# Kernel tuning notes

Measured on AMD Instinct MI355X. Metric: run time of the kernel, lower is better.

Reference implementation:

```python
import jax, jax.numpy as jnp
import numpy as np

B, T, I, H, K, C, TH, CLS = 128, 512, 300, 150, 6, 300, 20, 5

def setup_inputs() -> dict:
    key = jax.random.key(0)
    ks = jax.random.split(key, 16)
    s = lambda *sh: 1.0 / np.sqrt(sh[-1])
    inp = {
        "x": jax.random.normal(ks[0], (B, T, I), jnp.float32),
        # GRU params (PyTorch layout: [3H, in]) for fwd/bwd directions
        "Wih_f": jax.random.normal(ks[1], (3 * H, I), jnp.float32) * s(3 * H, I),
        "Whh_f": jax.random.normal(ks[2], (3 * H, H), jnp.float32) * s(3 * H, H),
        "bih_f": jax.random.normal(ks[3], (3 * H,), jnp.float32) * 0.01,
        "bhh_f": jax.random.normal(ks[4], (3 * H,), jnp.float32) * 0.01,
        "Wih_b": jax.random.normal(ks[5], (3 * H, I), jnp.float32) * s(3 * H, I),
        "Whh_b": jax.random.normal(ks[6], (3 * H, H), jnp.float32) * s(3 * H, H),
        "bih_b": jax.random.normal(ks[7], (3 * H,), jnp.float32) * 0.01,
        "bhh_b": jax.random.normal(ks[8], (3 * H,), jnp.float32) * 0.01,
        # topic attention params (stacked over K topics)
        "attn_context": jax.random.normal(ks[9], (K, C), jnp.float32),
        "Wattn": jax.random.normal(ks[10], (K, C + 2 * H, 2 * H), jnp.float32) * s(1, C + 2 * H),
        "battn": jax.random.normal(ks[11], (K, 2 * H), jnp.float32) * 0.01,
        "Wtop": jax.random.normal(ks[12], (K, 2 * H, TH), jnp.float32) * s(1, 2 * H),
        "btop": jax.random.normal(ks[13], (K, TH), jnp.float32) * 0.01,
        "Wout": jax.random.normal(ks[14], (K * TH, CLS), jnp.float32) * s(1, K * TH),
        "bout": jax.random.normal(ks[15], (CLS,), jnp.float32) * 0.01,
    }
    return inp

def _gru_dir(x, Wih, Whh, bih, bhh, reverse):
    # x: [B,T,I] -> outputs [B,T,H], final hidden [B,H]
    xT = jnp.swapaxes(x, 0, 1)                    # [T,B,I]
    if reverse:
        xT = xT[::-1]
    gi = xT @ Wih.T + bih                         # [T,B,3H] input projections (one big GEMM)
    h0 = jnp.zeros((x.shape[0], Whh.shape[1]), x.dtype)
    def step(h, g):
        gh = h @ Whh.T + bhh
        i_r, i_z, i_n = jnp.split(g, 3, axis=-1)
        h_r, h_z, h_n = jnp.split(gh, 3, axis=-1)
        r = jax.nn.sigmoid(i_r + h_r)
        z = jax.nn.sigmoid(i_z + h_z)
        n = jnp.tanh(i_n + r * h_n)
        h_new = (1.0 - z) * n + z * h
        return h_new, h_new
    hT, ys = jax.lax.scan(step, h0, gi)
    if reverse:
        ys = ys[::-1]
    return jnp.swapaxes(ys, 0, 1), hT

def reference(x, Wih_f, Whh_f, bih_f, bhh_f, Wih_b, Whh_b, bih_b, bhh_b,
              attn_context, Wattn, battn, Wtop, btop, Wout, bout):
    # eval mode: dropout is identity
    out_f, h_f = _gru_dir(x, Wih_f, Whh_f, bih_f, bhh_f, False)
    out_b, h_b = _gru_dir(x, Wih_b, Whh_b, bih_b, bhh_b, True)
    seq = jnp.concatenate([out_f, out_b], axis=-1)       # [B,T,2H]
    hidden = jnp.concatenate([h_f, h_b], axis=-1)        # [B,2H]
    Bsz = x.shape[0]
    Kt = attn_context.shape[0]
    # per-topic context: cat(context_k, hidden) -> linear -> tanh, batched over topics
    ctx_in = jnp.concatenate([
        jnp.broadcast_to(attn_context[None, :, :], (Bsz, Kt, attn_context.shape[1])),
        jnp.broadcast_to(hidden[:, None, :], (Bsz, Kt, hidden.shape[1])),
    ], axis=-1)                                          # [B,K,C+2H]
    context = jnp.tanh(jnp.einsum('bkc,kcd->bkd', ctx_in, Wattn) + battn)  # [B,K,2H]
    # attention pooling over time, all topics at once
    energy = jnp.einsum('btd,bkd->btk', seq, context)    # [B,T,K]
    probs = jax.nn.softmax(energy, axis=1)
    pooled = jnp.einsum('btd,btk->bkd', seq, probs)      # [B,K,2H]
    topic = jax.nn.relu(jnp.einsum('bkd,kdh->bkh', pooled, Wtop) + btop)   # [B,K,TH]
    feats = topic.reshape(Bsz, -1)                       # [B,K*TH]
    logits = feats @ Wout + bout
    out = jax.nn.softmax(logits, axis=1)                 # eval + validate=False path
    # regularization loss on normalized contexts
    nc = context / jnp.linalg.norm(context, axis=2, keepdims=True).clip(1e-12)
    G = jnp.einsum('bkd,bjd->bkj', nc, nc)               # [B,K,K]
    diff = G - jnp.eye(Kt, dtype=G.dtype)[None]
    reg = jnp.mean(jnp.sqrt(jnp.sum(diff * diff, axis=(1, 2))))
    return out, reg
```

## Files before the change

### kernel.cpp

```cpp
#include <hip/hip_runtime.h>
#include <hip/hip_bf16.h>
#include <math.h>

#define Bq   128
#define Tq   512
#define Iq   300
#define Hq   150
#define G3   450
#define Kq   6
#define Cq   300
#define D2   300
#define THq  20
#define CLSq 5

typedef __attribute__((ext_vector_type(8))) short short8;
typedef __attribute__((ext_vector_type(4))) float floatx4;

__global__ __launch_bounds__(256) void cast_bf16_kernel(
    const float* __restrict__ in, __hip_bfloat16* __restrict__ out, int n4)
{
    const int i = blockIdx.x * 256 + threadIdx.x;
    if (i < n4) {
        float4 v = *(const float4*)(in + 4 * (size_t)i);
        out[4 * (size_t)i + 0] = __float2bfloat16(v.x);
        out[4 * (size_t)i + 1] = __float2bfloat16(v.y);
        out[4 * (size_t)i + 2] = __float2bfloat16(v.z);
        out[4 * (size_t)i + 3] = __float2bfloat16(v.w);
    }
}

#define LB 40

__global__ __launch_bounds__(256) void gi_gemm_mfma(
    const __hip_bfloat16* __restrict__ xb,
    const __hip_bfloat16* __restrict__ Wbf,
    const float* __restrict__ bf_, const float* __restrict__ bb_,
    float* __restrict__ gic, int t0f, int t0b, int tcShift)
{
    const int dir = blockIdx.z;
    const unsigned short* W = (const unsigned short*)(Wbf + (size_t)dir * G3 * Iq);
    const unsigned short* X = (const unsigned short*)xb;
    const float* bias = dir ? bb_ : bf_;
    const int t0 = dir ? t0b : t0f;
    const int TCr = 1 << tcShift;
    float* outb = gic + (size_t)dir * Bq * TCr * G3;

    const int m0 = blockIdx.y * 128;
    const int n0 = blockIdx.x * 128;
    const int tid  = threadIdx.x;
    const int wv   = tid >> 6, lane = tid & 63;
    const int wm   = wv & 1,  wn   = wv >> 1;
    const int quad = lane >> 4, mr = lane & 15;

    __shared__ __align__(16) unsigned short Ab[128 * LB];
    __shared__ __align__(16) unsigned short Bb[128 * LB];

    floatx4 acc[4][4];
    #pragma unroll
    for (int i = 0; i < 4; ++i)
        #pragma unroll
        for (int j = 0; j < 4; ++j)
            acc[i][j] = (floatx4){0.f, 0.f, 0.f, 0.f};

    for (int k0 = 0; k0 < 320; k0 += 32) {
        __syncthreads();
        #pragma unroll
        for (int i = 0; i < 4; ++i) {
            const int g = tid + 256 * i;
            const int row = g >> 3, kq = g & 7;
            const int k = k0 + kq * 4;
            const int r = m0 + row;
            const int bb2 = r >> tcShift, lt = r & (TCr - 1);
            ushort4 av = make_ushort4(0, 0, 0, 0);
            if (k < Iq)
                av = *(const ushort4*)(X + ((size_t)bb2 * Tq + t0 + lt) * Iq + k);
            *(ushort4*)&Ab[row * LB + kq * 4] = av;
            const int n = n0 + row;
            ushort4 bv = make_ushort4(0, 0, 0, 0);
            if (n < G3 && k < Iq)
                bv = *(const ushort4*)(W + (size_t)n * Iq + k);
            *(ushort4*)&Bb[row * LB + kq * 4] = bv;
        }
        __syncthreads();

        short8 af[4], bfr[4];
        #pragma unroll
        for (int i = 0; i < 4; ++i)
            af[i] = *(const short8*)&Ab[(wm * 64 + i * 16 + mr) * LB + quad * 8];
        #pragma unroll
        for (int j = 0; j < 4; ++j)
            bfr[j] = *(const short8*)&Bb[(wn * 64 + j * 16 + mr) * LB + quad * 8];
        #pragma unroll
        for (int i = 0; i < 4; ++i)
            #pragma unroll
            for (int j = 0; j < 4; ++j)
                acc[i][j] = __builtin_amdgcn_mfma_f32_16x16x32_bf16(
                    af[i], bfr[j], acc[i][j], 0, 0, 0);
    }

    #pragma unroll
    for (int j = 0; j < 4; ++j) {
        const int gn = n0 + wn * 64 + j * 16 + mr;
        if (gn >= G3) continue;
        const float bv = bias[gn];
        #pragma unroll
        for (int i = 0; i < 4; ++i) {
            const int mbase = m0 + wm * 64 + i * 16 + quad * 4;
            #pragma unroll
            for (int rg = 0; rg < 4; ++rg)
                outb[(size_t)(mbase + rg) * G3 + gn] = acc[i][j][rg] + bv;
        }
    }
}

__global__ __launch_bounds__(512, 2) void gru_rec(
    const float* __restrict__ gic,
    const float* __restrict__ Whh_f, const float* __restrict__ bhh_f,
    const float* __restrict__ Whh_b, const float* __restrict__ bhh_b,
    float* __restrict__ hstate,
    float* __restrict__ seq,
    int chunk, int tcShift)
{
    const int TCr = 1 << tcShift;
    const int bid = blockIdx.x;
    const int dir = bid & 1;
    const int b   = bid >> 1;
    const float* Whh = dir ? Whh_b : Whh_f;
    const float* bhh = dir ? bhh_b : bhh_f;
    const int tid = threadIdx.x;
    const int j2  = tid >> 1;
    const int p   = tid & 1;
    const bool gact = (tid < 450);

    __shared__ __align__(16) float stage[64 * 150];
    __shared__ __align__(16) float4 hbuf4[38];
    __shared__ float gh_s[456];
    __shared__ float gi_s[456];
    float* hbuf = (float*)hbuf4;

    float w0[76], w1[76];

    for (int c = 0; c < 8; ++c) {
        const int r0 = c * 64;
        const int nrows = (r0 + 64 <= G3) ? 64 : (G3 - r0);
        const int nel = nrows * 150;
        __syncthreads();
        for (int idx = tid * 4; idx < nel; idx += 512 * 4)
            *(float4*)&stage[idx] = *(const float4*)(Whh + (size_t)r0 * 150 + idx);
        __syncthreads();
        if (gact && (j2 >> 5) == c) {
            const int rl = 2 * j2 - r0;
            #pragma unroll
            for (int m = 0; m < 75; ++m) {
                w0[m] = stage[rl * 150 + p * 75 + m];
                w1[m] = stage[(rl + 1) * 150 + p * 75 + m];
            }
        }
    }
    w0[75] = 0.f; w1[75] = 0.f;
    const float bh0 = (gact && p == 0) ? bhh[2 * j2]     : 0.f;
    const float bh1 = (gact && p == 0) ? bhh[2 * j2 + 1] : 0.f;

    float* hs = hstate + (size_t)(dir * Bq + b) * Hq;
    if (tid < 152) {
        const int pp = tid / 76, mm = tid % 76;
        hbuf[tid] = (mm < 75 && chunk > 0) ? hs[pp * 75 + mm] : 0.f;
    }
    __syncthreads();

    const float* gib = gic + (size_t)(dir * Bq + b) * TCr * G3;
    const int t0 = dir ? (Tq - TCr * (chunk + 1)) : (chunk * TCr);
    float* seqb = seq + (size_t)b * Tq * D2 + dir * Hq;

    int lt = dir ? (TCr - 1) : 0;
    float gval = gact ? gib[(size_t)lt * G3 + tid] : 0.f;

    for (int s = 0; s < TCr; ++s) {
        const int ltn = dir ? (TCr - 2 - s) : (s + 1);
        float gnext = 0.f;
        if (s + 1 < TCr && gact)
            gnext = gib[(size_t)ltn * G3 + tid];

        if (gact) {
            float a0a = 0.f, a0b = 0.f, a1a = 0.f, a1b = 0.f;
            const float4* hh = hbuf4 + p * 19;
            #pragma unroll
            for (int q = 0; q < 19; q += 2) {
                float4 hv = hh[q];
                a0a += hv.x * w0[q*4+0] + hv.y * w0[q*4+1]
                     + hv.z * w0[q*4+2] + hv.w * w0[q*4+3];
                a1a += hv.x * w1[q*4+0] + hv.y * w1[q*4+1]
                     + hv.z * w1[q*4+2] + hv.w * w1[q*4+3];
            }
            #pragma unroll
            for (int q = 1; q < 19; q += 2) {
                float4 hv = hh[q];
                a0b += hv.x * w0[q*4+0] + hv.y * w0[q*4+1]
                     + hv.z * w0[q*4+2] + hv.w * w0[q*4+3];
                a1b += hv.x * w1[q*4+0] + hv.y * w1[q*4+1]
                     + hv.z * w1[q*4+2] + hv.w * w1[q*4+3];
            }
            float acc0 = a0a + a0b, acc1 = a1a + a1b;
            const float o0 = __shfl_xor(acc0, 1);
            const float o1 = __shfl_xor(acc1, 1);
            if (p == 0)
                *(float2*)&gh_s[2 * j2] = make_float2(acc0 + o0 + bh0,
                                                      acc1 + o1 + bh1);
            gi_s[tid] = gval;
        }
        __syncthreads();

        if (tid < Hq) {
            const float r = 1.f / (1.f + __expf(-(gi_s[tid]       + gh_s[tid])));
            const float z = 1.f / (1.f + __expf(-(gi_s[150 + tid] + gh_s[150 + tid])));
            const float nv = tanhf(gi_s[300 + tid] + r * gh_s[300 + tid]);
            const int slot = (tid / 75) * 76 + (tid % 75);
            const float hn = (1.f - z) * nv + z * hbuf[slot];
            hbuf[slot] = hn;
            stage[(s & 63) * 150 + tid] = hn;
        }
        __syncthreads();

        if ((s & 63) == 63 || s == TCr - 1) {
            const int sf0 = s & ~63;
            const int nf2 = (s - sf0 + 1) * 75;
            for (int idx = tid; idx < nf2; idx += 512) {
                const int rrow = idx / 75, cc = idx % 75;
                const int ss = sf0 + rrow;
                const int ltw = dir ? (TCr - 1 - ss) : ss;
                *(float2*)(seqb + (size_t)(t0 + ltw) * D2 + 2 * cc) =
                    *(const float2*)&stage[rrow * 150 + 2 * cc];
            }
        }

        gval = gnext;
        lt = ltn;
    }

    if (tid < Hq) hs[tid] = hbuf[(tid / 75) * 76 + (tid % 75)];
}

__global__ void ctxw_kernel(
    const float* __restrict__ attn_context,
    const float* __restrict__ Wattn,
    const float* __restrict__ battn,
    float* __restrict__ ctxW)
{
    const int o = blockIdx.x * 256 + threadIdx.x;
    if (o >= Kq * D2) return;
    const int k = o / D2, d = o % D2;
    float acc = battn[o];
    const float* Wp = Wattn + ((size_t)k * (Cq + D2)) * D2 + d;
    for (int c = 0; c < Cq; ++c)
        acc += attn_context[k * Cq + c] * Wp[(size_t)c * D2];
    ctxW[o] = acc;
}

__global__ __launch_bounds__(256) void ctx_compute(
    const float* __restrict__ seq,
    const float* __restrict__ Wattn,
    const float* __restrict__ ctxW,
    float* __restrict__ context,
    float* __restrict__ normsq)
{
    const int b = blockIdx.x;
    const int k = blockIdx.y;
    const int tid = threadIdx.x;
    const int lane = tid & 63, wv = tid >> 6;

    __shared__ float hb[304];
    __shared__ float red[4];

    for (int i = tid; i < D2; i += 256)
        hb[i] = (i < Hq) ? seq[((size_t)b * Tq + (Tq - 1)) * D2 + i]
                         : seq[(size_t)b * Tq * D2 + i];
    __syncthreads();

    float ssq = 0.f;
    for (int d = tid; d < D2; d += 256) {
        float acc = ctxW[k * D2 + d];
        const float* Wp = Wattn + ((size_t)k * (Cq + D2) + Cq) * D2 + d;
        for (int jj = 0; jj < D2; ++jj)
            acc += hb[jj] * Wp[(size_t)jj * D2];
        const float c = tanhf(acc);
        context[((size_t)b * Kq + k) * D2 + d] = c;
        ssq += c * c;
    }
    for (int off = 32; off > 0; off >>= 1) ssq += __shfl_xor(ssq, off, 64);
    if (lane == 0) red[wv] = ssq;
    __syncthreads();
    if (tid == 0) normsq[b * Kq + k] = red[0] + red[1] + red[2] + red[3];
}

__global__ __launch_bounds__(256) void gram_kernel(
    const float* __restrict__ context,
    const float* __restrict__ normsq,
    float* __restrict__ regbuf)
{
    const int b = blockIdx.x;
    const int tid = threadIdx.x;
    __shared__ float ctx[Kq * D2];
    __shared__ float Gm[36];

    for (int o = tid; o < Kq * D2; o += 256)
        ctx[o] = context[(size_t)b * Kq * D2 + o];
    __syncthreads();

    if (tid < 36) {
        const int k = tid / 6, jj = tid % 6;
        float g = 0.f;
        for (int d = 0; d < D2; ++d)
            g += ctx[k * D2 + d] * ctx[jj * D2 + d];
        const float nk = fmaxf(sqrtf(normsq[b * Kq + k]), 1e-12f);
        const float nj = fmaxf(sqrtf(normsq[b * Kq + jj]), 1e-12f);
        g /= (nk * nj);
        const float diff = g - ((k == jj) ? 1.f : 0.f);
        Gm[tid] = diff * diff;
    }
    __syncthreads();
    if (tid == 0) {
        float s = 0.f;
        for (int i = 0; i < 36; ++i) s += Gm[i];
        regbuf[b] = sqrtf(s);
    }
}

__global__ __launch_bounds__(256) void energy_kernel(
    const float* __restrict__ seq,
    const float* __restrict__ context,
    float* __restrict__ en)
{
    const int tc = blockIdx.x;
    const int b  = blockIdx.y;
    const int tid = threadIdx.x;
    const int lane = tid & 63, wv = tid >> 6;

    __shared__ float ctx[Kq * D2];
    for (int o = tid; o < Kq * D2; o += 256)
        ctx[o] = context[(size_t)b * Kq * D2 + o];
    __syncthreads();

    const float* seqb = seq + (size_t)b * Tq * D2;
    for (int s = 0; s < 16; ++s) {
        const int tt = tc * 64 + s * 4 + wv;
        float acc[Kq] = {0.f,0.f,0.f,0.f,0.f,0.f};
        for (int d = lane; d < D2; d += 64) {
            const float sv = seqb[(size_t)tt * D2 + d];
            #pragma unroll
            for (int k = 0; k < Kq; ++k) acc[k] += sv * ctx[k * D2 + d];
        }
        #pragma unroll
        for (int k = 0; k < Kq; ++k) {
            float v = acc[k];
            for (int off = 32; off > 0; off >>= 1) v += __shfl_xor(v, off, 64);
            if (lane == 0) en[((size_t)b * Tq + tt) * Kq + k] = v;
        }
    }
}

__global__ __launch_bounds__(256) void softmax_kernel(float* __restrict__ en)
{
    const int b = blockIdx.x;
    const int tid = threadIdx.x;
    const int lane = tid & 63, wv = tid >> 6;
    __shared__ float es[Tq * Kq];
    __shared__ float red[8];

    for (int o = tid; o < Tq * Kq; o += 256)
        es[o] = en[(size_t)b * Tq * Kq + o];
    __syncthreads();

    for (int k = 0; k < Kq; ++k) {
        float m = -1e30f;
        for (int tt = tid; tt < Tq; tt += 256) m = fmaxf(m, es[tt * Kq + k]);
        for (int off = 32; off > 0; off >>= 1) m = fmaxf(m, __shfl_xor(m, off, 64));
        if (lane == 0) red[wv] = m;
        __syncthreads();
        m = fmaxf(fmaxf(red[0], red[1]), fmaxf(red[2], red[3]));
        float ssum = 0.f;
        for (int tt = tid; tt < Tq; tt += 256) {
            const float e = __expf(es[tt * Kq + k] - m);
            es[tt * Kq + k] = e;
            ssum += e;
        }
        for (int off = 32; off > 0; off >>= 1) ssum += __shfl_xor(ssum, off, 64);
        if (lane == 0) red[4 + wv] = ssum;
        __syncthreads();
        const float inv = 1.f / (red[4] + red[5] + red[6] + red[7]);
        for (int tt = tid; tt < Tq; tt += 256) es[tt * Kq + k] *= inv;
        __syncthreads();
    }

    for (int o = tid; o < Tq * Kq; o += 256)
        en[(size_t)b * Tq * Kq + o] = es[o];
}

__global__ __launch_bounds__(256) void pooledp_kernel(
    const float* __restrict__ seq,
    const float* __restrict__ en,
    float* __restrict__ partial)
{
    const int tc = blockIdx.x;
    const int b  = blockIdx.y;
    const int tid = threadIdx.x;
    const int lane = tid & 63, wv = tid >> 6;

    __shared__ float pr[64 * Kq];
    __shared__ float part[4][Kq * D2];

    if (tid < 64 * Kq / 2) {
        pr[tid]       = en[((size_t)b * Tq + tc * 64) * Kq + tid];
        pr[tid + 192] = en[((size_t)b * Tq + tc * 64) * Kq + tid + 192];
    }
    __syncthreads();

    const float* seqb = seq + (size_t)b * Tq * D2;

    float pp[Kq][5];
    #pragma unroll
    for (int k = 0; k < Kq; ++k)
        #pragma unroll
        for (int q = 0; q < 5; ++q) pp[k][q] = 0.f;

    for (int s = 0; s < 16; ++s) {
        const int tl = s * 4 + wv;
        const int tt = tc * 64 + tl;
        float prr[Kq];
        #pragma unroll
        for (int k = 0; k < Kq; ++k) prr[k] = pr[tl * Kq + k];
        #pragma unroll
        for (int q = 0; q < 5; ++q) {
            const int d = lane + q * 64;
            const float sv = (d < D2) ? seqb[(size_t)tt * D2 + d] : 0.f;
            #pragma unroll
            for (int k = 0; k < Kq; ++k) pp[k][q] += prr[k] * sv;
        }
    }
    #pragma unroll
    for (int k = 0; k < Kq; ++k)
        #pragma unroll
        for (int q = 0; q < 5; ++q) {
            const int d = lane + q * 64;
            if (d < D2) part[wv][k * D2 + d] = pp[k][q];
        }
    __syncthreads();
    float* op = partial + ((size_t)b * 8 + tc) * (Kq * D2);
    for (int o = tid; o < Kq * D2; o += 256)
        op[o] = part[0][o] + part[1][o] + part[2][o] + part[3][o];
}

__global__ __launch_bounds__(256) void final_kernel(
    const float* __restrict__ partial,
    const float* __restrict__ Wtop,
    const float* __restrict__ btop,
    const float* __restrict__ Wout,
    const float* __restrict__ bout,
    float* __restrict__ outp)
{
    const int b = blockIdx.x;
    const int tid = threadIdx.x;
    __shared__ float pooled[Kq * D2];
    __shared__ float feats[Kq * THq];
    __shared__ float lsm[8];

    for (int o = tid; o < Kq * D2; o += 256) {
        float s = 0.f;
        #pragma unroll
        for (int c = 0; c < 8; ++c)
            s += partial[((size_t)b * 8 + c) * (Kq * D2) + o];
        pooled[o] = s;
    }
    __syncthreads();

    if (tid < Kq * THq) {
        const int k = tid / THq, hh = tid % THq;
        float acc = btop[tid];
        const float* wp = Wtop + (size_t)k * D2 * THq + hh;
        for (int d = 0; d < D2; ++d)
            acc += pooled[k * D2 + d] * wp[(size_t)d * THq];
        feats[tid] = fmaxf(acc, 0.f);
    }
    __syncthreads();

    if (tid < CLSq) {
        float acc = bout[tid];
        for (int f = 0; f < Kq * THq; ++f)
            acc += feats[f] * Wout[f * CLSq + tid];
        lsm[tid] = acc;
    }
    __syncthreads();
    if (tid < CLSq) {
        float m = lsm[0];
        for (int c = 1; c < CLSq; ++c) m = fmaxf(m, lsm[c]);
        float s = 0.f;
        for (int c = 0; c < CLSq; ++c) s += __expf(lsm[c] - m);
        outp[(size_t)b * CLSq + tid] = __expf(lsm[tid] - m) / s;
    }
}

__global__ void reg_final(const float* __restrict__ regbuf, float* __restrict__ outp)
{
    const int tid = threadIdx.x;
    float v = regbuf[tid];
    for (int off = 32; off > 0; off >>= 1) v += __shfl_xor(v, off, 64);
    __shared__ float r2[2];
    if ((tid & 63) == 0) r2[tid >> 6] = v;
    __syncthreads();
    if (tid == 0) outp[Bq * CLSq] = (r2[0] + r2[1]) * (1.f / (float)Bq);
}

extern "C" void kernel_launch(void* const* d_in, const int* in_sizes, int n_in,
                              void* d_out, int out_size, void* d_ws, size_t ws_size,
                              hipStream_t stream)
{
    const float* x     = (const float*)d_in[0];
    const float* Wih_f = (const float*)d_in[1];
    const float* Whh_f = (const float*)d_in[2];
    const float* bih_f = (const float*)d_in[3];
    const float* bhh_f = (const float*)d_in[4];
    const float* Wih_b = (const float*)d_in[5];
    const float* Whh_b = (const float*)d_in[6];
    const float* bih_b = (const float*)d_in[7];
    const float* bhh_b = (const float*)d_in[8];
    const float* attn_context = (const float*)d_in[9];
    const float* Wattn = (const float*)d_in[10];
    const float* battn = (const float*)d_in[11];
    const float* Wtop  = (const float*)d_in[12];
    const float* btop  = (const float*)d_in[13];
    const float* Wout  = (const float*)d_in[14];
    const float* bout  = (const float*)d_in[15];
    float* outp = (float*)d_out;

    float* ws       = (float*)d_ws;
    float* seqv     = ws;
    float* hstate   = seqv + (size_t)Bq * Tq * D2;
    float* ctxW     = hstate + (size_t)2 * Bq * Hq;
    float* context  = ctxW + Kq * D2;
    float* regbuf   = context + (size_t)Bq * Kq * D2;
    float* normsq   = regbuf + Bq;
    float* en       = normsq + Bq * Kq;
    float* partial  = en + (size_t)Bq * Tq * Kq;
    __hip_bfloat16* xb16 = (__hip_bfloat16*)(partial + (size_t)Bq * 8 * Kq * D2);
    __hip_bfloat16* Wb16 = xb16 + (size_t)Bq * Tq * Iq;
    float* gi_chunk = (float*)(Wb16 + (size_t)2 * G3 * Iq);
    const size_t fixed_floats = (size_t)(gi_chunk - ws);

    int tcShift = 5;
    for (int sh = 8; sh >= 5; --sh) {
        size_t need = (fixed_floats + (size_t)115200 * (1 << sh)) * 4;
        if (need <= ws_size) { tcShift = sh; break; }
    }
    const int TCr = 1 << tcShift;
    const int NL = Tq / TCr;

    cast_bf16_kernel<<<dim3((Bq * Tq * Iq / 4 + 255) / 256), 256, 0, stream>>>(
        x, xb16, Bq * Tq * Iq / 4);
    cast_bf16_kernel<<<dim3((G3 * Iq / 4 + 255) / 256), 256, 0, stream>>>(
        Wih_f, Wb16, G3 * Iq / 4);
    cast_bf16_kernel<<<dim3((G3 * Iq / 4 + 255) / 256), 256, 0, stream>>>(
        Wih_b, Wb16 + (size_t)G3 * Iq, G3 * Iq / 4);

    for (int c = 0; c < NL; ++c) {
        const int t0f = c * TCr;
        const int t0b = Tq - TCr * (c + 1);
        gi_gemm_mfma<<<dim3(4, Bq * TCr / 128, 2), 256, 0, stream>>>(
            xb16, Wb16, bih_f, bih_b, gi_chunk, t0f, t0b, tcShift);
        gru_rec<<<dim3(2 * Bq), 512, 0, stream>>>(
            gi_chunk, Whh_f, bhh_f, Whh_b, bhh_b, hstate, seqv, c, tcShift);
    }

    ctxw_kernel<<<dim3((Kq * D2 + 255) / 256), 256, 0, stream>>>(
        attn_context, Wattn, battn, ctxW);
    ctx_compute<<<dim3(Bq, Kq), 256, 0, stream>>>(seqv, Wattn, ctxW, context, normsq);
    gram_kernel<<<dim3(Bq), 256, 0, stream>>>(context, normsq, regbuf);
    energy_kernel<<<dim3(8, Bq), 256, 0, stream>>>(seqv, context, en);
    softmax_kernel<<<dim3(Bq), 256, 0, stream>>>(en);
    pooledp_kernel<<<dim3(8, Bq), 256, 0, stream>>>(seqv, en, partial);
    final_kernel<<<dim3(Bq), 256, 0, stream>>>(partial, Wtop, btop, Wout, bout, outp);
    reg_final<<<dim3(1), 128, 0, stream>>>(regbuf, outp);
}
```

Before: 1.065 ms.

## Repartition GRU recurrent matvec to 8 rows x 8 column slices per thread

The recurrent h·Whh^T matvec is redistributed so each thread owns 8 gate rows over a 19-element column slice, in place of 2 rows over 75 columns. Each thread now reads 5 float4s of h from shared memory per step instead of 19, cutting LDS traffic. The cost is a 3-stage xor-shuffle reduction across 8 lanes for 8 accumulators. The hidden-state buffer layout is padded to 8 slices of 20 to match.

```diff
diff --git a/kernel.cpp b/kernel.cpp
--- a/kernel.cpp
+++ b/kernel.cpp
@@ -128,17 +128,18 @@
     const float* Whh = dir ? Whh_b : Whh_f;
     const float* bhh = dir ? bhh_b : bhh_f;
     const int tid = threadIdx.x;
-    const int j2  = tid >> 1;
-    const int p   = tid & 1;
-    const bool gact = (tid < 450);
+    const int ro  = tid >> 3;
+    const int p   = tid & 7;
+    const bool gact = (tid < 456);
+    const bool iact = (tid < 450);
 
     __shared__ __align__(16) float stage[64 * 150];
-    __shared__ __align__(16) float4 hbuf4[38];
-    __shared__ float gh_s[456];
+    __shared__ __align__(16) float4 hbuf4[40];
+    __shared__ __align__(16) float gh_s[456];
     __shared__ float gi_s[456];
     float* hbuf = (float*)hbuf4;
 
-    float w0[76], w1[76];
+    float w[8][19];
 
     for (int c = 0; c < 8; ++c) {
         const int r0 = c * 64;
@@ -148,23 +149,29 @@
         for (int idx = tid * 4; idx < nel; idx += 512 * 4)
             *(float4*)&stage[idx] = *(const float4*)(Whh + (size_t)r0 * 150 + idx);
         __syncthreads();
-        if (gact && (j2 >> 5) == c) {
-            const int rl = 2 * j2 - r0;
-            #pragma unroll
-            for (int m = 0; m < 75; ++m) {
-                w0[m] = stage[rl * 150 + p * 75 + m];
-                w1[m] = stage[(rl + 1) * 150 + p * 75 + m];
+        if (gact && (ro >> 3) == c) {
+            const int rl = 8 * ro - r0;
+            const int cmax = (p == 7) ? 17 : 19;
+            #pragma unroll
+            for (int r = 0; r < 8; ++r) {
+                const bool rv = (8 * ro + r < G3) && (rl + r < nrows);
+                #pragma unroll
+                for (int cc = 0; cc < 19; ++cc)
+                    w[r][cc] = (rv && cc < cmax)
+                             ? stage[(rl + r) * 150 + p * 19 + cc] : 0.f;
             }
         }
     }
-    w0[75] = 0.f; w1[75] = 0.f;
-    const float bh0 = (gact && p == 0) ? bhh[2 * j2]     : 0.f;
-    const float bh1 = (gact && p == 0) ? bhh[2 * j2 + 1] : 0.f;
+    float bh[8];
+    #pragma unroll
+    for (int r = 0; r < 8; ++r)
+        bh[r] = (gact && p == 0 && 8 * ro + r < G3) ? bhh[8 * ro + r] : 0.f;
 
     float* hs = hstate + (size_t)(dir * Bq + b) * Hq;
-    if (tid < 152) {
-        const int pp = tid / 76, mm = tid % 76;
-        hbuf[tid] = (mm < 75 && chunk > 0) ? hs[pp * 75 + mm] : 0.f;
+    if (tid < 160) {
+        const int pp = tid / 20, off = tid % 20;
+        const int j = pp * 19 + off;
+        hbuf[tid] = (off < 19 && j < Hq && chunk > 0) ? hs[j] : 0.f;
     }
     __syncthreads();
 
@@ -173,40 +180,49 @@
     float* seqb = seq + (size_t)b * Tq * D2 + dir * Hq;
 
     int lt = dir ? (TCr - 1) : 0;
-    float gval = gact ? gib[(size_t)lt * G3 + tid] : 0.f;
+    float gval = iact ? gib[(size_t)lt * G3 + tid] : 0.f;
 
     for (int s = 0; s < TCr; ++s) {
         const int ltn = dir ? (TCr - 2 - s) : (s + 1);
         float gnext = 0.f;
-        if (s + 1 < TCr && gact)
+        if (s + 1 < TCr && iact)
             gnext = gib[(size_t)ltn * G3 + tid];
 
+        if (iact) gi_s[tid] = gval;
+
         if (gact) {
-            float a0a = 0.f, a0b = 0.f, a1a = 0.f, a1b = 0.f;
-            const float4* hh = hbuf4 + p * 19;
-            #pragma unroll
-            for (int q = 0; q < 19; q += 2) {
-                float4 hv = hh[q];
-                a0a += hv.x * w0[q*4+0] + hv.y * w0[q*4+1]
-                     + hv.z * w0[q*4+2] + hv.w * w0[q*4+3];
-                a1a += hv.x * w1[q*4+0] + hv.y * w1[q*4+1]
-                     + hv.z * w1[q*4+2] + hv.w * w1[q*4+3];
+            const float4 hv0 = hbuf4[p * 5 + 0];
+            const float4 hv1 = hbuf4[p * 5 + 1];
+            const float4 hv2 = hbuf4[p * 5 + 2];
+            const float4 hv3 = hbuf4[p * 5 + 3];
+            const float4 hv4 = hbuf4[p * 5 + 4];
+            float acc[8];
+            #pragma unroll
+            for (int r = 0; r < 8; ++r) {
+                acc[r] = hv0.x * w[r][0]  + hv0.y * w[r][1]
+                       + hv0.z * w[r][2]  + hv0.w * w[r][3]
+                       + hv1.x * w[r][4]  + hv1.y * w[r][5]
+                       + hv1.z * w[r][6]  + hv1.w * w[r][7]
+                       + hv2.x * w[r][8]  + hv2.y * w[r][9]
+                       + hv2.z * w[r][10] + hv2.w * w[r][11]
+                       + hv3.x * w[r][12] + hv3.y * w[r][13]
+                       + hv3.z * w[r][14] + hv3.w * w[r][15]
+                       + hv4.x * w[r][16] + hv4.y * w[r][17]
+                       + hv4.z * w[r][18];
             }
             #pragma unroll
-            for (int q = 1; q < 19; q += 2) {
-                float4 hv = hh[q];
-                a0b += hv.x * w0[q*4+0] + hv.y * w0[q*4+1]
-                     + hv.z * w0[q*4+2] + hv.w * w0[q*4+3];
-                a1b += hv.x * w1[q*4+0] + hv.y * w1[q*4+1]
-                     + hv.z * w1[q*4+2] + hv.w * w1[q*4+3];
+            for (int m = 1; m < 8; m <<= 1)
+                #pragma unroll
+                for (int r = 0; r < 8; ++r)
+                    acc[r] += __shfl_xor(acc[r], m);
+            if (p == 0) {
+                float4 lo = make_float4(acc[0] + bh[0], acc[1] + bh[1],
+                                        acc[2] + bh[2], acc[3] + bh[3]);
+                float4 hi = make_float4(acc[4] + bh[4], acc[5] + bh[5],
+                                        acc[6] + bh[6], acc[7] + bh[7]);
+                *(float4*)&gh_s[8 * ro]     = lo;
+                *(float4*)&gh_s[8 * ro + 4] = hi;
             }
-            float acc0 = a0a + a0b, acc1 = a1a + a1b;
-            const float o0 = __shfl_xor(acc0, 1);
-            const float o1 = __shfl_xor(acc1, 1);
-            if (p == 0)
-                *(float2*)&gh_s[2 * j2] = make_float2(acc0 + o0 + bh0,
-                                                      acc1 + o1 + bh1);
-            gi_s[tid] = gval;
         }
         __syncthreads();
 
@@ -214,7 +230,7 @@
             const float r = 1.f / (1.f + __expf(-(gi_s[tid]       + gh_s[tid])));
             const float z = 1.f / (1.f + __expf(-(gi_s[150 + tid] + gh_s[150 + tid])));
             const float nv = tanhf(gi_s[300 + tid] + r * gh_s[300 + tid]);
-            const int slot = (tid / 75) * 76 + (tid % 75);
+            const int slot = (tid / 19) * 20 + (tid % 19);
             const float hn = (1.f - z) * nv + z * hbuf[slot];
             hbuf[slot] = hn;
             stage[(s & 63) * 150 + tid] = hn;
@@ -237,7 +253,7 @@
         lt = ltn;
     }
 
-    if (tid < Hq) hs[tid] = hbuf[(tid / 75) * 76 + (tid % 75)];
+    if (tid < Hq) hs[tid] = hbuf[(tid / 19) * 20 + (tid % 19)];
 }
 
 __global__ void ctxw_kernel(
```

After: 1.196 ms. 1.12x slower.

## Split GRU recurrent matvec into 4 rows by 4 column-quarters per thread

Applied to the files above, without the earlier changes.

Changes the recurrent matvec mapping from 2 rows by half the hidden dimension per thread to 4 rows by a quarter of the hidden dimension per thread, so each thread still holds 160 weight registers. Partial sums go to four shared buffers and are reduced in the gate step, which replaces the cross-lane shuffle. Each float4 hidden-state load now feeds four rows instead of two, cutting LDS reads per FMA. The cost is more shared-memory traffic for the partial sums, fewer active threads (452), and padding work in the last column block.

```diff
diff --git a/kernel.cpp b/kernel.cpp
--- a/kernel.cpp
+++ b/kernel.cpp
@@ -128,17 +128,18 @@
     const float* Whh = dir ? Whh_b : Whh_f;
     const float* bhh = dir ? bhh_b : bhh_f;
     const int tid = threadIdx.x;
-    const int j2  = tid >> 1;
-    const int p   = tid & 1;
-    const bool gact = (tid < 450);
+    const int rq  = tid >> 2;
+    const int p   = tid & 3;
+    const bool gact = (rq < 113);
+    const bool iact = (tid < 450);
 
     __shared__ __align__(16) float stage[64 * 150];
-    __shared__ __align__(16) float4 hbuf4[38];
-    __shared__ float gh_s[456];
+    __shared__ __align__(16) float4 hbuf4[40];
+    __shared__ __align__(16) float ghp[4][456];
     __shared__ float gi_s[456];
     float* hbuf = (float*)hbuf4;
 
-    float w0[76], w1[76];
+    float w[4][40];
 
     for (int c = 0; c < 8; ++c) {
         const int r0 = c * 64;
@@ -148,23 +149,33 @@
         for (int idx = tid * 4; idx < nel; idx += 512 * 4)
             *(float4*)&stage[idx] = *(const float4*)(Whh + (size_t)r0 * 150 + idx);
         __syncthreads();
-        if (gact && (j2 >> 5) == c) {
-            const int rl = 2 * j2 - r0;
+        if (gact && (rq >> 4) == c) {
+            const int rl = 4 * rq - r0;
+            const int cmax = (p == 3) ? 36 : 38;
             #pragma unroll
-            for (int m = 0; m < 75; ++m) {
-                w0[m] = stage[rl * 150 + p * 75 + m];
-                w1[m] = stage[(rl + 1) * 150 + p * 75 + m];
+            for (int r = 0; r < 4; ++r) {
+                const bool rv = (4 * rq + r < G3);
+                #pragma unroll
+                for (int cc = 0; cc < 40; ++cc)
+                    w[r][cc] = (rv && cc < cmax)
+                             ? stage[(rl + r) * 150 + p * 38 + cc] : 0.f;
             }
         }
     }
-    w0[75] = 0.f; w1[75] = 0.f;
-    const float bh0 = (gact && p == 0) ? bhh[2 * j2]     : 0.f;
-    const float bh1 = (gact && p == 0) ? bhh[2 * j2 + 1] : 0.f;
+
+    float bh3[3] = {0.f, 0.f, 0.f};
+    if (tid < Hq) {
+        bh3[0] = bhh[tid];
+        bh3[1] = bhh[150 + tid];
+        bh3[2] = bhh[300 + tid];
+    }
+    const int hslot = (tid / 38) * 40 + (tid % 38);
 
     float* hs = hstate + (size_t)(dir * Bq + b) * Hq;
-    if (tid < 152) {
-        const int pp = tid / 76, mm = tid % 76;
-        hbuf[tid] = (mm < 75 && chunk > 0) ? hs[pp * 75 + mm] : 0.f;
+    if (tid < 160) {
+        const int pp = tid / 40, off = tid % 40;
+        const int j = pp * 38 + off;
+        hbuf[tid] = (off < 38 && j < Hq && chunk > 0) ? hs[j] : 0.f;
     }
     __syncthreads();
 
@@ -173,50 +184,47 @@
     float* seqb = seq + (size_t)b * Tq * D2 + dir * Hq;
 
     int lt = dir ? (TCr - 1) : 0;
-    float gval = gact ? gib[(size_t)lt * G3 + tid] : 0.f;
+    float gval = iact ? gib[(size_t)lt * G3 + tid] : 0.f;
 
     for (int s = 0; s < TCr; ++s) {
         const int ltn = dir ? (TCr - 2 - s) : (s + 1);
         float gnext = 0.f;
-        if (s + 1 < TCr && gact)
+        if (s + 1 < TCr && iact)
             gnext = gib[(size_t)ltn * G3 + tid];
 
+        if (iact) gi_s[tid] = gval;
+
         if (gact) {
-            float a0a = 0.f, a0b = 0.f, a1a = 0.f, a1b = 0.f;
-            const float4* hh = hbuf4 + p * 19;
+            const float4* hh = hbuf4 + p * 10;
+            float acc0 = 0.f, acc1 = 0.f, acc2 = 0.f, acc3 = 0.f;
             #pragma unroll
-            for (int q = 0; q < 19; q += 2) {
-                float4 hv = hh[q];
-                a0a += hv.x * w0[q*4+0] + hv.y * w0[q*4+1]
-                     + hv.z * w0[q*4+2] + hv.w * w0[q*4+3];
-                a1a += hv.x * w1[q*4+0] + hv.y * w1[q*4+1]
-                     + hv.z * w1[q*4+2] + hv.w * w1[q*4+3];
+            for (int q = 0; q < 10; ++q) {
+                const float4 hv = hh[q];
+                acc0 += hv.x * w[0][4*q]   + hv.y * w[0][4*q+1]
+                      + hv.z * w[0][4*q+2] + hv.w * w[0][4*q+3];
+                acc1 += hv.x * w[1][4*q]   + hv.y * w[1][4*q+1]
+                      + hv.z * w[1][4*q+2] + hv.w * w[1][4*q+3];
+                acc2 += hv.x * w[2][4*q]   + hv.y * w[2][4*q+1]
+                      + hv.z * w[2][4*q+2] + hv.w * w[2][4*q+3];
+                acc3 += hv.x * w[3][4*q]   + hv.y * w[3][4*q+1]
+                      + hv.z * w[3][4*q+2] + hv.w * w[3][4*q+3];
             }
-            #pragma unroll
-            for (int q = 1; q < 19; q += 2) {
-                float4 hv = hh[q];
-                a0b += hv.x * w0[q*4+0] + hv.y * w0[q*4+1]
-                     + hv.z * w0[q*4+2] + hv.w * w0[q*4+3];
-                a1b += hv.x * w1[q*4+0] + hv.y * w1[q*4+1]
-                     + hv.z * w1[q*4+2] + hv.w * w1[q*4+3];
-            }
-            float acc0 = a0a + a0b, acc1 = a1a + a1b;
-            const float o0 = __shfl_xor(acc0, 1);
-            const float o1 = __shfl_xor(acc1, 1);
-            if (p == 0)
-                *(float2*)&gh_s[2 * j2] = make_float2(acc0 + o0 + bh0,
-                                                      acc1 + o1 + bh1);
-            gi_s[tid] = gval;
+            *(float4*)&ghp[p][4 * rq] = make_float4(acc0, acc1, acc2, acc3);
         }
         __syncthreads();
 
         if (tid < Hq) {
-            const float r = 1.f / (1.f + __expf(-(gi_s[tid]       + gh_s[tid])));
-            const float z = 1.f / (1.f + __expf(-(gi_s[150 + tid] + gh_s[150 + tid])));
-            const float nv = tanhf(gi_s[300 + tid] + r * gh_s[300 + tid]);
-            const int slot = (tid / 75) * 76 + (tid % 75);
-            const float hn = (1.f - z) * nv + z * hbuf[slot];
-            hbuf[slot] = hn;
+            const float ghr = ghp[0][tid] + ghp[1][tid]
+                            + ghp[2][tid] + ghp[3][tid] + bh3[0];
+            const float ghz = ghp[0][150+tid] + ghp[1][150+tid]
+                            + ghp[2][150+tid] + ghp[3][150+tid] + bh3[1];
+            const float ghn = ghp[0][300+tid] + ghp[1][300+tid]
+                            + ghp[2][300+tid] + ghp[3][300+tid] + bh3[2];
+            const float r = 1.f / (1.f + __expf(-(gi_s[tid]       + ghr)));
+            const float z = 1.f / (1.f + __expf(-(gi_s[150 + tid] + ghz)));
+            const float nv = tanhf(gi_s[300 + tid] + r * ghn);
+            const float hn = (1.f - z) * nv + z * hbuf[hslot];
+            hbuf[hslot] = hn;
             stage[(s & 63) * 150 + tid] = hn;
         }
         __syncthreads();
@@ -237,7 +245,7 @@
         lt = ltn;
     }
 
-    if (tid < Hq) hs[tid] = hbuf[(tid / 75) * 76 + (tid % 75)];
+    if (tid < Hq) hs[tid] = hbuf[hslot];
 }
 
 __global__ void ctxw_kernel(
```

New measurement: 1.047 ms. No clear change (-1.7%).
